# Optimization experiments

Measured on AMD Instinct MI355X. Metric: run time of the kernel, lower is better.

Reference implementation:

```python
import jax, jax.numpy as jnp
import numpy as np

NUM_NODES = 100000
NUM_EDGES = 2500000
NUM_GRAPHS = 512
IN_DIM = 14
HID = 32
N_EXTRA_CONVS = 4  # num_layers - 1


def setup_inputs() -> dict:
    key = jax.random.key(0)
    ks = jax.random.split(key, 16)
    x = jax.random.normal(ks[0], (NUM_NODES, IN_DIM), dtype=jnp.float32)
    edge_index = jax.random.randint(ks[1], (2, NUM_EDGES), 0, NUM_NODES, dtype=jnp.int64)
    batch = jnp.sort(jax.random.randint(ks[2], (NUM_NODES,), 0, NUM_GRAPHS, dtype=jnp.int64))
    s = 1.0 / np.sqrt(HID)
    # PyG GraphConv: out = lin_rel(aggr_add(x_j)) + lin_root(x_i); lin_rel has bias, lin_root has no bias
    W_rel1 = jax.random.uniform(ks[3], (IN_DIM, HID), jnp.float32, -s, s)
    b_rel1 = jax.random.uniform(ks[4], (HID,), jnp.float32, -s, s)
    W_root1 = jax.random.uniform(ks[5], (IN_DIM, HID), jnp.float32, -s, s)
    W_rel = jax.random.uniform(ks[6], (N_EXTRA_CONVS, HID, HID), jnp.float32, -s, s)
    b_rel = jax.random.uniform(ks[7], (N_EXTRA_CONVS, HID), jnp.float32, -s, s)
    W_root = jax.random.uniform(ks[8], (N_EXTRA_CONVS, HID, HID), jnp.float32, -s, s)
    lin1_w = jax.random.uniform(ks[9], (HID, HID), jnp.float32, -s, s)
    lin1_b = jax.random.uniform(ks[10], (HID,), jnp.float32, -s, s)
    lin2_w = jax.random.uniform(ks[11], (HID, 2), jnp.float32, -s, s)
    lin2_b = jax.random.uniform(ks[12], (2,), jnp.float32, -s, s)
    return {
        "x": x, "W_rel1": W_rel1, "b_rel1": b_rel1, "W_root1": W_root1,
        "W_rel": W_rel, "b_rel": b_rel, "W_root": W_root,
        "lin1_w": lin1_w, "lin1_b": lin1_b, "lin2_w": lin2_w, "lin2_b": lin2_b,
        "edge_index": edge_index, "batch": batch,
    }


def reference(x, W_rel1, b_rel1, W_root1, W_rel, b_rel, W_root,
              lin1_w, lin1_b, lin2_w, lin2_b, edge_index, batch):
    src, dst = edge_index[0], edge_index[1]

    def graph_conv(h, wr, br, wroot):
        # sum-aggregate neighbor features: scatter-add messages h[src] into dst
        agg = jax.ops.segment_sum(h[src], dst, num_segments=NUM_NODES)
        return agg @ wr + br + h @ wroot

    h = jax.nn.relu(graph_conv(x, W_rel1, b_rel1, W_root1))
    for i in range(N_EXTRA_CONVS):
        h = jax.nn.relu(graph_conv(h, W_rel[i], b_rel[i], W_root[i]))
    # sum pooling per graph
    g = jax.ops.segment_sum(h, batch, num_segments=NUM_GRAPHS)
    g = jax.nn.relu(g @ lin1_w + lin1_b)
    # dropout is identity in eval mode
    logits = g @ lin2_w + lin2_b
    return jax.nn.log_softmax(logits, axis=1)
```

## Files before the change

### kernel.cpp

```cpp
#include <hip/hip_runtime.h>
#include <math.h>

#define N_NODES 100000
#define N_EDGES 2500000
#define N_GRAPHS 512
#define IN_DIM 14
#define HID 32
#define CAP 64

#define BSHIFT 7
#define BNODES 128
#define NB 782
#define NBP 784
#define NBANKS 8
#define SUBCAP 512
#define BCAP 4096
#define CHUNK 4096
#define TB_BIN 1024
#define NBLK_E ((N_EDGES + CHUNK - 1) / CHUNK)
#define EPT (CHUNK / TB_BIN)
#define PX_BLKS 400
#define TB_BS 512

#define GSTRIDE 8
#define GCUR_N (NBP * NBANKS * GSTRIDE)

typedef unsigned int uint;
typedef unsigned short ushort;
typedef float v2f __attribute__((ext_vector_type(2)));

__device__ inline float bflo(uint w) { return __uint_as_float(w << 16); }
__device__ inline float bfhi(uint w) { return __uint_as_float(w & 0xffff0000u); }
__device__ inline ushort f2bf(float f) {
    uint u = __float_as_uint(f);
    return (ushort)((u + 0x7fffu + ((u >> 16) & 1u)) >> 16);
}

__global__ __launch_bounds__(1024)
void bin_or_pad(const int* __restrict__ src, const int* __restrict__ dst,
                int* __restrict__ gcur, int* __restrict__ binned,
                const float* __restrict__ x, ushort* __restrict__ x16,
                uint2* __restrict__ f0, uint2* __restrict__ f1) {
    __shared__ int scnt[NBP];
    __shared__ int sbase[NBP];
    int t = threadIdx.x;

    if (blockIdx.x >= NBLK_E) {
        int pj = blockIdx.x - NBLK_E;
        if (pj == 0) {
            if (t < 2) ((uint4*)(x16 + (size_t)N_NODES * 16))[t] = make_uint4(0, 0, 0, 0);
            else if (t < 6) f0[(size_t)N_NODES * 4 + (t - 2)] = make_uint2(0, 0);
            else if (t < 10) f1[(size_t)N_NODES * 4 + (t - 6)] = make_uint2(0, 0);
        }
#pragma unroll
        for (int k = 0; k < 4; ++k) {
            int idx = pj * 4096 + k * 1024 + t;
            if (idx < N_NODES * 16) {
                int n = idx >> 4, kk = idx & 15;
                x16[idx] = (kk < IN_DIM) ? f2bf(x[(size_t)n * IN_DIM + kk]) : (ushort)0;
            }
        }
        return;
    }

    for (int i = t; i < NBP; i += TB_BIN) scnt[i] = 0;
    __syncthreads();
    int base = blockIdx.x * CHUNK;
    int bank = blockIdx.x & (NBANKS - 1);
    int dreg[EPT];
    int rreg[EPT];
#pragma unroll
    for (int j = 0; j < EPT; ++j) {
        int e = base + j * TB_BIN + t;
        dreg[j] = (e < N_EDGES) ? __builtin_nontemporal_load(dst + e) : -1;
        rreg[j] = (dreg[j] >= 0) ? atomicAdd(&scnt[dreg[j] >> BSHIFT], 1) : 0;
    }
    __syncthreads();
    if (t < NBP) {
        int c = scnt[t];
        sbase[t] = (c > 0) ? atomicAdd(&gcur[(bank * NBP + t) * GSTRIDE], c) : 0;
    }
    __syncthreads();
#pragma unroll
    for (int j = 0; j < EPT; ++j) {
        int d = dreg[j];
        if (d >= 0) {
            int e = base + j * TB_BIN + t;
            int b = d >> BSHIFT;
            int s = __builtin_nontemporal_load(src + e);
            int pos = sbase[b] + rreg[j];
            if (pos < SUBCAP)
                binned[b * BCAP + bank * SUBCAP + pos] = (s << BSHIFT) | (d & (BNODES - 1));
        }
    }
}

__global__ __launch_bounds__(TB_BS)
void build_slots(const int* __restrict__ gcur, const int* __restrict__ binned,
                 int* __restrict__ deg, int* __restrict__ slots) {
    __shared__ int stile[BNODES * CAP];
    __shared__ int sdeg[BNODES];
    int t = threadIdx.x;
    for (int i = t; i < BNODES * CAP; i += TB_BS) stile[i] = N_NODES;
    if (t < BNODES) sdeg[t] = 0;
    __syncthreads();
    int b = blockIdx.x;
#pragma unroll
    for (int k = 0; k < NBANKS; ++k) {
        int cnt = gcur[(k * NBP + b) * GSTRIDE]; if (cnt > SUBCAP) cnt = SUBCAP;
        const int* seg = binned + b * BCAP + k * SUBCAP;
        for (int i = t; i < cnt; i += TB_BS) {
            int w = __builtin_nontemporal_load(seg + i);
            int ld = w & (BNODES - 1), sn = w >> BSHIFT;
            int p = atomicAdd(&sdeg[ld], 1);
            if (p < CAP) stile[ld * CAP + p] = sn;
        }
    }
    __syncthreads();
    int nbase = b * BNODES;
    int rows = N_NODES - nbase; if (rows > BNODES) rows = BNODES;
    int r = t & 127, h = t >> 7;
    if (r < rows) {
        int dv = sdeg[r]; if (dv > CAP) dv = CAP;
        if (h == 0) deg[nbase + r] = dv;
        int n4 = ((dv + 15) >> 4) << 2;
        int4* drow = (int4*)(slots + (size_t)(nbase + r) * CAP);
        const int4* srow = (const int4*)(stile + r * CAP);
        for (int i = h; i < n4; i += 4) drow[i] = srow[i];
    }
}

__global__ __launch_bounds__(256, 6)
void conv1_fused(const int* __restrict__ deg, const int* __restrict__ slots,
                 const ushort* __restrict__ x16,
                 const float* __restrict__ Wrel,
                 const float* __restrict__ bias,
                 const float* __restrict__ Wroot,
                 uint2* __restrict__ outf8) {
    __shared__ float sWrel[16 * HID];
    __shared__ float sWroot[16 * HID];
    __shared__ float sb[HID];
    int t = threadIdx.x;
    for (int i = t; i < 16 * HID; i += 256) {
        sWrel[i]  = (i < IN_DIM * HID) ? Wrel[i] : 0.f;
        sWroot[i] = (i < IN_DIM * HID) ? Wroot[i] : 0.f;
    }
    if (t < HID) sb[t] = bias[t];
    __syncthreads();

    int n = blockIdx.x * 64 + (t >> 2);
    if (n >= N_NODES) return;
    int q = t & 3;

    int dn = __builtin_nontemporal_load(deg + n); if (dn > CAP) dn = CAP;
    int rounds = (dn + 7) >> 3;
    const int* sl = slots + (size_t)n * CAP;
    int2 my[8];
#pragma unroll
    for (int r = 0; r < 8; ++r)
        if (r < rounds) {
            long w = __builtin_nontemporal_load((const long*)(sl + r * 8 + q * 2));
            my[r].x = (int)(w & 0xffffffffL);
            my[r].y = (int)(w >> 32);
        }

    v2f a2[2] = {{0.f, 0.f}, {0.f, 0.f}};
#pragma unroll
    for (int r = 0; r < 8; ++r) {
        if (r < rounds) {
#pragma unroll
            for (int j = 0; j < 8; ++j) {
                int c = __shfl((j & 1) ? my[r].y : my[r].x, j >> 1, 4);
                uint2 v = *(const uint2*)(x16 + (size_t)c * 16 + q * 4);
                a2[0] += (v2f){bflo(v.x), bfhi(v.x)};
                a2[1] += (v2f){bflo(v.y), bfhi(v.y)};
            }
        }
    }
    float a[4] = {a2[0].x, a2[0].y, a2[1].x, a2[1].y};

    float r8[8];
#pragma unroll
    for (int o = 0; o < 8; ++o) r8[o] = sb[q * 8 + o];

#pragma unroll
    for (int cl = 0; cl < 4; ++cl) {
#pragma unroll
        for (int j = 0; j < 4; ++j) {
            float av = __shfl(a[j], cl, 4);
            const float* w = &sWrel[(cl * 4 + j) * HID + q * 8];
#pragma unroll
            for (int o = 0; o < 8; ++o) r8[o] += av * w[o];
        }
    }

    uint2 h2 = *(const uint2*)(x16 + (size_t)n * 16 + q * 4);
    float hh[4] = {bflo(h2.x), bfhi(h2.x), bflo(h2.y), bfhi(h2.y)};
#pragma unroll
    for (int cl = 0; cl < 4; ++cl) {
#pragma unroll
        for (int j = 0; j < 4; ++j) {
            float hv = __shfl(hh[j], cl, 4);
            const float* w = &sWroot[(cl * 4 + j) * HID + q * 8];
#pragma unroll
            for (int o = 0; o < 8; ++o) r8[o] += hv * w[o];
        }
    }

    float v[8];
#pragma unroll
    for (int o = 0; o < 8; ++o) v[o] = fmaxf(r8[o], 0.f);

    uint w0 = __builtin_amdgcn_cvt_pk_bf8_f32(v[0], v[1], 0u, false);
    w0 = __builtin_amdgcn_cvt_pk_bf8_f32(v[2], v[3], w0, true);
    uint w1 = __builtin_amdgcn_cvt_pk_bf8_f32(v[4], v[5], 0u, false);
    w1 = __builtin_amdgcn_cvt_pk_bf8_f32(v[6], v[7], w1, true);
    outf8[(size_t)n * 4 + q] = make_uint2(w0, w1);
}

template <bool WRITE_B16, bool WRITE_F8>
__global__ __launch_bounds__(256, 6)
void conv_bf8(const int* __restrict__ deg, const int* __restrict__ slots,
              const uint2* __restrict__ gat,
              const float* __restrict__ Wrel,
              const float* __restrict__ bias,
              const float* __restrict__ Wroot,
              ushort* __restrict__ outb,
              uint2* __restrict__ outf8) {
    __shared__ float sWrel[HID * HID];
    __shared__ float sWroot[HID * HID];
    __shared__ float sb[HID];
    int t = threadIdx.x;
    for (int i = t; i < HID * HID; i += 256) { sWrel[i] = Wrel[i]; sWroot[i] = Wroot[i]; }
    if (t < HID) sb[t] = bias[t];
    __syncthreads();

    int n = blockIdx.x * 64 + (t >> 2);
    if (n >= N_NODES) return;
    int q = t & 3;

    int dn = __builtin_nontemporal_load(deg + n); if (dn > CAP) dn = CAP;
    int rounds = (dn + 7) >> 3;
    const int* sl = slots + (size_t)n * CAP;
    int2 my[8];
#pragma unroll
    for (int r = 0; r < 8; ++r)
        if (r < rounds) {
            long w = __builtin_nontemporal_load((const long*)(sl + r * 8 + q * 2));
            my[r].x = (int)(w & 0xffffffffL);
            my[r].y = (int)(w >> 32);
        }

    float a[8] = {0.f, 0.f, 0.f, 0.f, 0.f, 0.f, 0.f, 0.f};
#pragma unroll
    for (int r = 0; r < 8; ++r) {
        if (r < rounds) {
#pragma unroll
            for (int j = 0; j < 8; ++j) {
                int c = __shfl((j & 1) ? my[r].y : my[r].x, j >> 1, 4);
                uint2 v = gat[(size_t)c * 4 + q];
                v2f p0 = __builtin_amdgcn_cvt_pk_f32_bf8(v.x, false);
                v2f p1 = __builtin_amdgcn_cvt_pk_f32_bf8(v.x, true);
                v2f p2 = __builtin_amdgcn_cvt_pk_f32_bf8(v.y, false);
                v2f p3 = __builtin_amdgcn_cvt_pk_f32_bf8(v.y, true);
                a[0] += p0.x; a[1] += p0.y; a[2] += p1.x; a[3] += p1.y;
                a[4] += p2.x; a[5] += p2.y; a[6] += p3.x; a[7] += p3.y;
            }
        }
    }

    float r8[8];
#pragma unroll
    for (int o = 0; o < 8; ++o) r8[o] = sb[q * 8 + o];

#pragma unroll
    for (int cl = 0; cl < 4; ++cl) {
#pragma unroll
        for (int j = 0; j < 8; ++j) {
            float av = __shfl(a[j], cl, 4);
            const float* w = &sWrel[(cl * 8 + j) * HID + q * 8];
#pragma unroll
            for (int o = 0; o < 8; ++o) r8[o] += av * w[o];
        }
    }

    {
        uint2 hv2 = gat[(size_t)n * 4 + q];
        v2f p0 = __builtin_amdgcn_cvt_pk_f32_bf8(hv2.x, false);
        v2f p1 = __builtin_amdgcn_cvt_pk_f32_bf8(hv2.x, true);
        v2f p2 = __builtin_amdgcn_cvt_pk_f32_bf8(hv2.y, false);
        v2f p3 = __builtin_amdgcn_cvt_pk_f32_bf8(hv2.y, true);
        float hh[8] = {p0.x, p0.y, p1.x, p1.y, p2.x, p2.y, p3.x, p3.y};
#pragma unroll
        for (int cl = 0; cl < 4; ++cl) {
#pragma unroll
            for (int j = 0; j < 8; ++j) {
                float hv = __shfl(hh[j], cl, 4);
                const float* w = &sWroot[(cl * 8 + j) * HID + q * 8];
#pragma unroll
                for (int o = 0; o < 8; ++o) r8[o] += hv * w[o];
            }
        }
    }

    float v[8];
#pragma unroll
    for (int o = 0; o < 8; ++o) v[o] = fmaxf(r8[o], 0.f);

    if constexpr (WRITE_B16) {
        uint pw[4];
#pragma unroll
        for (int m = 0; m < 4; ++m)
            pw[m] = (uint)f2bf(v[2 * m]) | ((uint)f2bf(v[2 * m + 1]) << 16);
        *(uint4*)(outb + (size_t)n * HID + q * 8) = make_uint4(pw[0], pw[1], pw[2], pw[3]);
    }
    if constexpr (WRITE_F8) {
        uint w0 = __builtin_amdgcn_cvt_pk_bf8_f32(v[0], v[1], 0u, false);
        w0 = __builtin_amdgcn_cvt_pk_bf8_f32(v[2], v[3], w0, true);
        uint w1 = __builtin_amdgcn_cvt_pk_bf8_f32(v[4], v[5], 0u, false);
        w1 = __builtin_amdgcn_cvt_pk_bf8_f32(v[6], v[7], w1, true);
        outf8[(size_t)n * 4 + q] = make_uint2(w0, w1);
    }
}

__global__ __launch_bounds__(256) void pool_head(
        const ushort* __restrict__ h, const int* __restrict__ batch,
        const float* __restrict__ w1, const float* __restrict__ b1,
        const float* __restrict__ w2, const float* __restrict__ b2,
        float* __restrict__ out) {
    __shared__ float sW1[HID][HID];
    __shared__ float sb1[HID];
    __shared__ float sW2[HID][2];
    __shared__ float sacc[8][HID];
    __shared__ float sg[HID];
    __shared__ float sl[2][HID];
    int t = threadIdx.x;
    int gid = blockIdx.x;
    for (int i = t; i < HID * HID; i += 256) sW1[i / HID][i % HID] = w1[i];
    if (t < HID) sb1[t] = b1[t];
    if (t < HID * 2) sW2[t >> 1][t & 1] = w2[t];

    int lo = 0, hi = N_NODES;
    while (lo < hi) { int m = (lo + hi) >> 1; if (batch[m] < gid) lo = m + 1; else hi = m; }
    int s = lo;
    hi = N_NODES;
    while (lo < hi) { int m = (lo + hi) >> 1; if (batch[m] < gid + 1) lo = m + 1; else hi = m; }
    int e = lo;

    int f = t & 31, r = t >> 5;
    float acc = 0.f;
    for (int n = s + r; n < e; n += 8)
        acc += bflo((uint)h[(size_t)n * HID + f]);
    sacc[r][f] = acc;
    __syncthreads();
    if (t < HID) {
        float gv = 0.f;
#pragma unroll
        for (int rr = 0; rr < 8; ++rr) gv += sacc[rr][t];
        sg[t] = gv;
    }
    __syncthreads();
    if (t < HID) {
        float a = sb1[t];
#pragma unroll
        for (int k = 0; k < HID; ++k) a += sg[k] * sW1[k][t];
        a = fmaxf(a, 0.f);
        sl[0][t] = a * sW2[t][0];
        sl[1][t] = a * sW2[t][1];
    }
    __syncthreads();
    if (t == 0) {
        float l0 = b2[0], l1 = b2[1];
#pragma unroll
        for (int o = 0; o < HID; ++o) { l0 += sl[0][o]; l1 += sl[1][o]; }
        float m = fmaxf(l0, l1);
        float lse = m + logf(expf(l0 - m) + expf(l1 - m));
        out[gid * 2 + 0] = l0 - lse;
        out[gid * 2 + 1] = l1 - lse;
    }
}

extern "C" void kernel_launch(void* const* d_in, const int* in_sizes, int n_in,
                              void* d_out, int out_size, void* d_ws, size_t ws_size,
                              hipStream_t stream) {
    const float* x      = (const float*)d_in[0];
    const float* W_rel1 = (const float*)d_in[1];
    const float* b_rel1 = (const float*)d_in[2];
    const float* W_root1= (const float*)d_in[3];
    const float* W_rel  = (const float*)d_in[4];
    const float* b_rel  = (const float*)d_in[5];
    const float* W_root = (const float*)d_in[6];
    const float* lin1_w = (const float*)d_in[7];
    const float* lin1_b = (const float*)d_in[8];
    const float* lin2_w = (const float*)d_in[9];
    const float* lin2_b = (const float*)d_in[10];
    const int*   ei     = (const int*)d_in[11];
    const int*   batch  = (const int*)d_in[12];
    float* out = (float*)d_out;

    const int* src = ei;
    const int* dst = ei + N_EDGES;

    int*    gcur   = (int*)d_ws;
    int*    binned = gcur + GCUR_N;
    int*    deg    = binned + NB * BCAP;
    int*    slots  = deg + N_NODES + 32;
    ushort* B1b    = (ushort*)(slots + (size_t)N_NODES * CAP);
    uint2*  F0     = (uint2*)(B1b + (size_t)(N_NODES + 1) * HID);
    uint2*  F1     = F0 + (size_t)(N_NODES + 1) * 4;
    ushort* X16    = (ushort*)(F1 + (size_t)(N_NODES + 1) * 4);

    dim3 blk(256);
    dim3 grd_cv((N_NODES + 63) / 64);

    hipMemsetAsync(gcur, 0, GCUR_N * sizeof(int), stream);
    bin_or_pad<<<dim3(NBLK_E + PX_BLKS), dim3(TB_BIN), 0, stream>>>(
        src, dst, gcur, binned, x, X16, F0, F1);
    build_slots<<<dim3(NB), dim3(TB_BS), 0, stream>>>(gcur, binned, deg, slots);

    conv1_fused<<<grd_cv, blk, 0, stream>>>(deg, slots, X16, W_rel1, b_rel1,
                                            W_root1, F1);

    uint2* curf = F1;
    uint2* nxtf = F0;
    for (int i = 0; i < 3; ++i) {
        conv_bf8<false, true><<<grd_cv, blk, 0, stream>>>(
            deg, slots, curf, W_rel + i * HID * HID, b_rel + i * HID,
            W_root + i * HID * HID, nullptr, nxtf);
        uint2* tf = curf; curf = nxtf; nxtf = tf;
    }
    conv_bf8<true, false><<<grd_cv, blk, 0, stream>>>(
        deg, slots, curf, W_rel + 3 * HID * HID, b_rel + 3 * HID,
        W_root + 3 * HID * HID, B1b, nullptr);

    pool_head<<<dim3(N_GRAPHS), blk, 0, stream>>>(B1b, batch, lin1_w, lin1_b,
                                                  lin2_w, lin2_b, out);
}
```

Measured before the change: 283.4 us.

## Fuse slot building with first graph convolution using shared-memory neighbor tiles

Merges the build_slots and conv1_fused kernels into one kernel per 128-node bin. The first convolution reads neighbor indices directly from the shared-memory tile instead of re-reading the slots array from global memory, which saves a launch and a global round trip. The tile row stride is padded to 68 ints to reduce LDS bank conflicts. In exchange, blocks are coarser (782 blocks of 512 threads) and the larger LDS footprint may reduce occupancy.

Measured after the change: 278.5 us. About the same (-1.7%).

```diff
diff --git a/kernel.cpp b/kernel.cpp
--- a/kernel.cpp
+++ b/kernel.cpp
@@ -20,7 +20,8 @@
 #define NBLK_E ((N_EDGES + CHUNK - 1) / CHUNK)
 #define EPT (CHUNK / TB_BIN)
 #define PX_BLKS 400
-#define TB_BS 512
+#define TB_SC 512
+#define SSTR 68
 
 #define GSTRIDE 8
 #define GCUR_N (NBP * NBANKS * GSTRIDE)
@@ -95,74 +96,66 @@
     }
 }
 
-__global__ __launch_bounds__(TB_BS)
-void build_slots(const int* __restrict__ gcur, const int* __restrict__ binned,
-                 int* __restrict__ deg, int* __restrict__ slots) {
-    __shared__ int stile[BNODES * CAP];
-    __shared__ int sdeg[BNODES];
-    int t = threadIdx.x;
-    for (int i = t; i < BNODES * CAP; i += TB_BS) stile[i] = N_NODES;
-    if (t < BNODES) sdeg[t] = 0;
-    __syncthreads();
-    int b = blockIdx.x;
-#pragma unroll
-    for (int k = 0; k < NBANKS; ++k) {
-        int cnt = gcur[(k * NBP + b) * GSTRIDE]; if (cnt > SUBCAP) cnt = SUBCAP;
-        const int* seg = binned + b * BCAP + k * SUBCAP;
-        for (int i = t; i < cnt; i += TB_BS) {
-            int w = __builtin_nontemporal_load(seg + i);
-            int ld = w & (BNODES - 1), sn = w >> BSHIFT;
-            int p = atomicAdd(&sdeg[ld], 1);
-            if (p < CAP) stile[ld * CAP + p] = sn;
-        }
-    }
-    __syncthreads();
-    int nbase = b * BNODES;
-    int rows = N_NODES - nbase; if (rows > BNODES) rows = BNODES;
-    int r = t & 127, h = t >> 7;
-    if (r < rows) {
-        int dv = sdeg[r]; if (dv > CAP) dv = CAP;
-        if (h == 0) deg[nbase + r] = dv;
-        int n4 = ((dv + 15) >> 4) << 2;
-        int4* drow = (int4*)(slots + (size_t)(nbase + r) * CAP);
-        const int4* srow = (const int4*)(stile + r * CAP);
-        for (int i = h; i < n4; i += 4) drow[i] = srow[i];
-    }
-}
-
-__global__ __launch_bounds__(256, 6)
-void conv1_fused(const int* __restrict__ deg, const int* __restrict__ slots,
+__global__ __launch_bounds__(TB_SC, 6)
+void slots_conv1(const int* __restrict__ gcur, const int* __restrict__ binned,
                  const ushort* __restrict__ x16,
                  const float* __restrict__ Wrel,
                  const float* __restrict__ bias,
                  const float* __restrict__ Wroot,
+                 int* __restrict__ deg, int* __restrict__ slots,
                  uint2* __restrict__ outf8) {
+    __shared__ int stile[BNODES * SSTR];
+    __shared__ int sdeg[BNODES];
     __shared__ float sWrel[16 * HID];
     __shared__ float sWroot[16 * HID];
     __shared__ float sb[HID];
     int t = threadIdx.x;
-    for (int i = t; i < 16 * HID; i += 256) {
+    for (int i = t; i < BNODES * SSTR; i += TB_SC) stile[i] = N_NODES;
+    if (t < BNODES) sdeg[t] = 0;
+    for (int i = t; i < 16 * HID; i += TB_SC) {
         sWrel[i]  = (i < IN_DIM * HID) ? Wrel[i] : 0.f;
         sWroot[i] = (i < IN_DIM * HID) ? Wroot[i] : 0.f;
     }
     if (t < HID) sb[t] = bias[t];
     __syncthreads();
-
-    int n = blockIdx.x * 64 + (t >> 2);
-    if (n >= N_NODES) return;
-    int q = t & 3;
-
-    int dn = __builtin_nontemporal_load(deg + n); if (dn > CAP) dn = CAP;
+    int b = blockIdx.x;
+#pragma unroll
+    for (int k = 0; k < NBANKS; ++k) {
+        int cnt = gcur[(k * NBP + b) * GSTRIDE]; if (cnt > SUBCAP) cnt = SUBCAP;
+        const int* seg = binned + b * BCAP + k * SUBCAP;
+        for (int i = t; i < cnt; i += TB_SC) {
+            int w = __builtin_nontemporal_load(seg + i);
+            int ld = w & (BNODES - 1), sn = w >> BSHIFT;
+            int p = atomicAdd(&sdeg[ld], 1);
+            if (p < CAP) stile[ld * SSTR + p] = sn;
+        }
+    }
+    __syncthreads();
+    int nbase = b * BNODES;
+    int rows = N_NODES - nbase; if (rows > BNODES) rows = BNODES;
+
+    {
+        int r = t & 127, h = t >> 7;
+        if (r < rows) {
+            int dv = sdeg[r]; if (dv > CAP) dv = CAP;
+            if (h == 0) deg[nbase + r] = dv;
+            int n4 = ((dv + 15) >> 4) << 2;
+            int4* drow = (int4*)(slots + (size_t)(nbase + r) * CAP);
+            const int4* srow = (const int4*)(stile + r * SSTR);
+            for (int i = h; i < n4; i += 4) drow[i] = srow[i];
+        }
+    }
+
+    int nl = t >> 2, q = t & 3;
+    if (nl >= rows) return;
+    int n = nbase + nl;
+    int dn = sdeg[nl]; if (dn > CAP) dn = CAP;
     int rounds = (dn + 7) >> 3;
-    const int* sl = slots + (size_t)n * CAP;
+    const int* slr = stile + nl * SSTR;
     int2 my[8];
 #pragma unroll
     for (int r = 0; r < 8; ++r)
-        if (r < rounds) {
-            long w = __builtin_nontemporal_load((const long*)(sl + r * 8 + q * 2));
-            my[r].x = (int)(w & 0xffffffffL);
-            my[r].y = (int)(w >> 32);
-        }
+        if (r < rounds) my[r] = *(const int2*)(slr + r * 8 + q * 2);
 
     v2f a2[2] = {{0.f, 0.f}, {0.f, 0.f}};
 #pragma unroll
@@ -416,10 +409,9 @@
     hipMemsetAsync(gcur, 0, GCUR_N * sizeof(int), stream);
     bin_or_pad<<<dim3(NBLK_E + PX_BLKS), dim3(TB_BIN), 0, stream>>>(
         src, dst, gcur, binned, x, X16, F0, F1);
-    build_slots<<<dim3(NB), dim3(TB_BS), 0, stream>>>(gcur, binned, deg, slots);
-
-    conv1_fused<<<grd_cv, blk, 0, stream>>>(deg, slots, X16, W_rel1, b_rel1,
-                                            W_root1, F1);
+
+    slots_conv1<<<dim3(NB), dim3(TB_SC), 0, stream>>>(
+        gcur, binned, X16, W_rel1, b_rel1, W_root1, deg, slots, F1);
 
     uint2* curf = F1;
     uint2* nxtf = F0;
```
